# Performance work log

Hardware: AMD Instinct MI355X
Metric: run time of the kernel (lower is better)

## Reference

```python
import jax, jax.numpy as jnp
import numpy as np

ALPHA = 0.01
EPS = 1e-15


def setup_inputs() -> dict:
    key = jax.random.key(0)
    k1, k2, k3, k4 = jax.random.split(key, 4)
    B, C = 65536, 1000
    out = jax.random.normal(k1, (B, C), dtype=jnp.float32)
    correction = jax.random.normal(k2, (C, C), dtype=jnp.float32)
    target = jax.random.randint(k3, (B,), 0, C, dtype=jnp.int64)
    T = jax.random.uniform(k4, (C, C), dtype=jnp.float32)
    return {"out": out, "correction": correction, "target": target, "T": T}


def reference(out, correction, target, T):
    # out: [B, C] logits; correction, T: [C, C]; target: [B]
    B = out.shape[0]
    rows = jnp.arange(B)

    log_p = jax.nn.log_softmax(out, axis=1)      # [B, C]
    p = jnp.exp(log_p)                           # softmax probs [B, C]

    # T_result = T + alpha * correction; out_T[i] = (T_result^T @ p[i]^T)^T = p[i] @ T_result
    T_result = T + ALPHA * correction            # [C, C]
    out_T = p @ T_result                         # [B, C]

    pro1 = p[rows, target]                       # [B]
    pro2 = out_T[rows, target]                   # [B]
    beta = jax.lax.stop_gradient(pro1 / (pro2 + EPS))  # detached reweight factor

    ce = -log_p[rows, target]                    # per-sample cross entropy [B]
    loss = jnp.mean(beta * ce)                   # sum(beta_i * ce_i) / B
    return loss
```

## Files before the change

kernel.cpp:

```cpp
#include <hip/hip_runtime.h>
#include <math.h>

#define ALPHA 0.01f
#define EPS 1e-15f

typedef float f32x4 __attribute__((ext_vector_type(4)));

__global__ __launch_bounds__(256) void build_TrT_kernel(
    const float* __restrict__ T, const float* __restrict__ corr,
    float* __restrict__ TrT, int C, float* __restrict__ out, int out_size) {
  if (blockIdx.x == 0 && blockIdx.y == 0 && threadIdx.y == 0) {
    for (int i = threadIdx.x; i < out_size; i += 32) out[i] = 0.f;
  }
  __shared__ float tile[32][33];
  const int bx = blockIdx.x * 32;
  const int by = blockIdx.y * 32;
  const int tx = threadIdx.x;
  for (int r = threadIdx.y; r < 32; r += blockDim.y) {
    int j = by + r;
    int t = bx + tx;
    if (j < C && t < C)
      tile[r][tx] = T[(size_t)j * C + t] + ALPHA * corr[(size_t)j * C + t];
  }
  __syncthreads();
  for (int r = threadIdx.y; r < 32; r += blockDim.y) {
    int t = bx + r;
    int j = by + tx;
    if (t < C && j < C)
      TrT[(size_t)t * C + j] = tile[tx][r];
  }
}

template <int CT>
__global__ __launch_bounds__(256) void loss_vec4_fast(
    const float* __restrict__ x, const int* __restrict__ target,
    const float* __restrict__ TrT, float* __restrict__ out,
    int B, float invB) {
  constexpr int F4 = CT / 4;
  constexpr int KF = F4 / 64;
  constexpr int REM = F4 - KF * 64;
  constexpr int KTOT = KF + (REM ? 1 : 0);

  const int lane = threadIdx.x & 63;
  const int wave = threadIdx.x >> 6;
  const int wpb = blockDim.x >> 6;
  const int gwave = blockIdx.x * wpb + wave;
  const int nwave = gridDim.x * wpb;

  float acc = 0.f;
  int row = gwave;
  int tnext = (row < B) ? target[row] : 0;
  for (; row < B; row += nwave) {
    const int t = tnext;
    {
      int nr = row + nwave;
      if (nr < B) tnext = target[nr];
    }
    const f32x4* xr = (const f32x4*)(x + (size_t)row * CT);
    const f32x4* tr = (const f32x4*)(TrT + (size_t)t * CT);
    const float xt = x[(size_t)row * CT + t];

    f32x4 v[KTOT], w[KTOT];
#pragma unroll
    for (int k = 0; k < KF; ++k) {
      const int idx = lane + 64 * k;
      v[k] = __builtin_nontemporal_load(xr + idx);
      w[k] = tr[idx];
    }
    if (REM) {
      const int idx = lane + 64 * KF;
      if (lane < REM) {
        v[KF] = __builtin_nontemporal_load(xr + idx);
        w[KF] = tr[idx];
      } else {
        v[KF] = f32x4{-INFINITY, -INFINITY, -INFINITY, -INFINITY};
        w[KF] = f32x4{0.f, 0.f, 0.f, 0.f};
      }
    }

    float se = 0.f, dot = 0.f;
#pragma unroll
    for (int k = 0; k < KTOT; ++k) {
      float e0 = __expf(v[k].x), e1 = __expf(v[k].y);
      float e2 = __expf(v[k].z), e3 = __expf(v[k].w);
      se += (e0 + e1) + (e2 + e3);
      dot += e0 * w[k].x + e1 * w[k].y + e2 * w[k].z + e3 * w[k].w;
    }
#pragma unroll
    for (int off = 32; off > 0; off >>= 1) {
      se += __shfl_xor(se, off, 64);
      dot += __shfl_xor(dot, off, 64);
    }

    const float et = __expf(xt);
    acc += (et / (dot + EPS * se)) * (__logf(se) - xt);
  }

  __shared__ float lacc[8];
  if (lane == 0) lacc[wave] = acc;
  __syncthreads();
  if (threadIdx.x == 0) {
    float s = 0.f;
    for (int i = 0; i < wpb; ++i) s += lacc[i];
    atomicAdd(out, s * invB);
  }
}

__global__ __launch_bounds__(256) void loss_generic_kernel(
    const float* __restrict__ x, const int* __restrict__ target,
    const float* __restrict__ TrT, const float* __restrict__ T,
    const float* __restrict__ corr, int useTrT,
    float* __restrict__ out, int B, int C, float invB) {
  const int lane = threadIdx.x & 63;
  const int wave = threadIdx.x >> 6;
  const int wpb = blockDim.x >> 6;
  const int gwave = blockIdx.x * wpb + wave;
  const int nwave = gridDim.x * wpb;

  float acc = 0.f;
  for (int row = gwave; row < B; row += nwave) {
    const float* xr = x + (size_t)row * C;
    float m = -INFINITY;
    for (int j = lane; j < C; j += 64) m = fmaxf(m, xr[j]);
#pragma unroll
    for (int off = 32; off > 0; off >>= 1) m = fmaxf(m, __shfl_xor(m, off, 64));

    const int t = target[row];
    const float* tr = TrT + (size_t)t * C;
    float se = 0.f, dot = 0.f;
    for (int j = lane; j < C; j += 64) {
      float e = __expf(xr[j] - m);
      float tv = useTrT ? tr[j]
                        : (T[(size_t)j * C + t] + ALPHA * corr[(size_t)j * C + t]);
      se += e;
      dot += e * tv;
    }
#pragma unroll
    for (int off = 32; off > 0; off >>= 1) {
      se += __shfl_xor(se, off, 64);
      dot += __shfl_xor(dot, off, 64);
    }

    const float xt = xr[t];
    const float et = __expf(xt - m);
    const float beta = (et / se) / (dot / se + EPS);
    const float ce = m + logf(se) - xt;
    acc += beta * ce;
  }

  __shared__ float lacc[8];
  if (lane == 0) lacc[wave] = acc;
  __syncthreads();
  if (threadIdx.x == 0) {
    float s = 0.f;
    for (int i = 0; i < wpb; ++i) s += lacc[i];
    atomicAdd(out, s * invB);
  }
}

extern "C" void kernel_launch(void* const* d_in, const int* in_sizes, int n_in,
                              void* d_out, int out_size, void* d_ws, size_t ws_size,
                              hipStream_t stream) {
  const float* logits = (const float*)d_in[0];
  const float* corr   = (const float*)d_in[1];
  const int*   target = (const int*)d_in[2];
  const float* T      = (const float*)d_in[3];

  const int B = in_sizes[2];
  const int C = in_sizes[0] / B;
  float* loss = (float*)d_out;

  float* TrT = (float*)d_ws;
  const bool useTrT = (ws_size >= (size_t)C * C * sizeof(float));
  const float invB = 1.0f / (float)B;
  const int blocks = 2048;

  if (useTrT && C == 1000) {
    dim3 tb(32, 8);
    dim3 tg((C + 31) / 32, (C + 31) / 32);
    build_TrT_kernel<<<tg, tb, 0, stream>>>(T, corr, TrT, C, loss, out_size);
    loss_vec4_fast<1000><<<blocks, 256, 0, stream>>>(logits, target, TrT, loss, B, invB);
  } else {
    hipMemsetAsync(d_out, 0, sizeof(float) * out_size, stream);
    if (useTrT) {
      dim3 tb(32, 8);
      dim3 tg((C + 31) / 32, (C + 31) / 32);
      build_TrT_kernel<<<tg, tb, 0, stream>>>(T, corr, TrT, C, loss, 0);
    }
    loss_generic_kernel<<<blocks, 256, 0, stream>>>(logits, target, TrT, T, corr,
                                                    useTrT ? 1 : 0, loss, B, C, invB);
  }
}
```

Before: 358.6 us.

## Bucket rows by target so each wave reuses one TrT row

```diff
diff --git a/kernel.cpp b/kernel.cpp
--- a/kernel.cpp
+++ b/kernel.cpp
@@ -3,39 +3,86 @@
 
 #define ALPHA 0.01f
 #define EPS 1e-15f
+#define CAP 1024
 
 typedef float f32x4 __attribute__((ext_vector_type(4)));
 
-__global__ __launch_bounds__(256) void build_TrT_kernel(
+
+__global__ __launch_bounds__(256) void build_TrT_init(
     const float* __restrict__ T, const float* __restrict__ corr,
-    float* __restrict__ TrT, int C, float* __restrict__ out, int out_size) {
-  if (blockIdx.x == 0 && blockIdx.y == 0 && threadIdx.y == 0) {
-    for (int i = threadIdx.x; i < out_size; i += 32) out[i] = 0.f;
+    float* __restrict__ TrT, int C, float* __restrict__ out, int out_size,
+    int* __restrict__ cursors, int nbuckets, int* __restrict__ ovf_cnt) {
+  if (blockIdx.x == 0 && blockIdx.y == 0) {
+    int tid = threadIdx.y * 32 + threadIdx.x;
+    for (int i = tid; i < nbuckets; i += 256) cursors[i] = 0;
+    for (int i = tid; i < out_size; i += 256) out[i] = 0.f;
+    if (tid == 0 && ovf_cnt) *ovf_cnt = 0;
   }
   __shared__ float tile[32][33];
-  const int bx = blockIdx.x * 32;
-  const int by = blockIdx.y * 32;
+  const int bx = blockIdx.x * 32, by = blockIdx.y * 32;
   const int tx = threadIdx.x;
   for (int r = threadIdx.y; r < 32; r += blockDim.y) {
-    int j = by + r;
-    int t = bx + tx;
+    int j = by + r, t = bx + tx;
     if (j < C && t < C)
       tile[r][tx] = T[(size_t)j * C + t] + ALPHA * corr[(size_t)j * C + t];
   }
   __syncthreads();
   for (int r = threadIdx.y; r < 32; r += blockDim.y) {
-    int t = bx + r;
-    int j = by + tx;
-    if (t < C && j < C)
-      TrT[(size_t)t * C + j] = tile[tx][r];
-  }
+    int t = bx + r, j = by + tx;
+    if (t < C && j < C) TrT[(size_t)t * C + j] = tile[tx][r];
+  }
+}
+
+__global__ __launch_bounds__(256) void scatter_kernel(
+    const int* __restrict__ target, int B, int* __restrict__ cursors,
+    int* __restrict__ rowlist, int* __restrict__ ovflist,
+    int* __restrict__ ovf_cnt) {
+  int i = blockIdx.x * 256 + threadIdx.x;
+  if (i >= B) return;
+  int t = target[i];
+  int k = atomicAdd(&cursors[t], 1);
+  if (k < CAP) rowlist[(size_t)t * CAP + k] = i;
+  else { int o = atomicAdd(ovf_cnt, 1); ovflist[o] = i; }
+}
+
+template <int CT, int KTOT, int KF, int REM>
+__device__ __forceinline__ float row_term(const float* __restrict__ x,
+                                          int row, int t, const f32x4* wv,
+                                          int lane) {
+  const f32x4* xr = (const f32x4*)(x + (size_t)row * CT);
+  const float xt = x[(size_t)row * CT + t];
+  f32x4 v[KTOT];
+#pragma unroll
+  for (int k = 0; k < KF; ++k)
+    v[k] = __builtin_nontemporal_load(xr + (lane + 64 * k));
+  if (REM) {
+    if (lane < REM) v[KF] = __builtin_nontemporal_load(xr + (lane + 64 * KF));
+    else v[KF] = f32x4{-INFINITY, -INFINITY, -INFINITY, -INFINITY};
+  }
+  float se = 0.f, dot = 0.f;
+#pragma unroll
+  for (int k = 0; k < KTOT; ++k) {
+    float e0 = __expf(v[k].x), e1 = __expf(v[k].y);
+    float e2 = __expf(v[k].z), e3 = __expf(v[k].w);
+    se += (e0 + e1) + (e2 + e3);
+    dot += e0 * wv[k].x + e1 * wv[k].y + e2 * wv[k].z + e3 * wv[k].w;
+  }
+#pragma unroll
+  for (int off = 32; off > 0; off >>= 1) {
+    se += __shfl_xor(se, off, 64);
+    dot += __shfl_xor(dot, off, 64);
+  }
+  const float et = __expf(xt);
+  return (et / (dot + EPS * se)) * (__logf(se) - xt);
 }
 
 template <int CT>
-__global__ __launch_bounds__(256) void loss_vec4_fast(
-    const float* __restrict__ x, const int* __restrict__ target,
-    const float* __restrict__ TrT, float* __restrict__ out,
-    int B, float invB) {
+__global__ __launch_bounds__(256) void loss_bucket(
+    const float* __restrict__ x, const float* __restrict__ TrT,
+    const int* __restrict__ cursors, const int* __restrict__ rowlist,
+    const int* __restrict__ ovflist, const int* __restrict__ ovf_cnt,
+    const int* __restrict__ target, float* __restrict__ out,
+    int nbuckets, float invB) {
   constexpr int F4 = CT / 4;
   constexpr int KF = F4 / 64;
   constexpr int REM = F4 - KF * 64;
@@ -44,65 +91,47 @@
   const int lane = threadIdx.x & 63;
   const int wave = threadIdx.x >> 6;
   const int wpb = blockDim.x >> 6;
-  const int gwave = blockIdx.x * wpb + wave;
-  const int nwave = gridDim.x * wpb;
+  const int gw = __builtin_amdgcn_readfirstlane(blockIdx.x * wpb + wave);
+  const int nw = gridDim.x * wpb;
 
   float acc = 0.f;
-  int row = gwave;
-  int tnext = (row < B) ? target[row] : 0;
-  for (; row < B; row += nwave) {
-    const int t = tnext;
-    {
-      int nr = row + nwave;
-      if (nr < B) tnext = target[nr];
-    }
-    const f32x4* xr = (const f32x4*)(x + (size_t)row * CT);
-    const f32x4* tr = (const f32x4*)(TrT + (size_t)t * CT);
-    const float xt = x[(size_t)row * CT + t];
-
-    f32x4 v[KTOT], w[KTOT];
-#pragma unroll
-    for (int k = 0; k < KF; ++k) {
-      const int idx = lane + 64 * k;
-      v[k] = __builtin_nontemporal_load(xr + idx);
-      w[k] = tr[idx];
-    }
-    if (REM) {
-      const int idx = lane + 64 * KF;
-      if (lane < REM) {
-        v[KF] = __builtin_nontemporal_load(xr + idx);
-        w[KF] = tr[idx];
-      } else {
-        v[KF] = f32x4{-INFINITY, -INFINITY, -INFINITY, -INFINITY};
-        w[KF] = f32x4{0.f, 0.f, 0.f, 0.f};
-      }
-    }
-
-    float se = 0.f, dot = 0.f;
-#pragma unroll
-    for (int k = 0; k < KTOT; ++k) {
-      float e0 = __expf(v[k].x), e1 = __expf(v[k].y);
-      float e2 = __expf(v[k].z), e3 = __expf(v[k].w);
-      se += (e0 + e1) + (e2 + e3);
-      dot += e0 * w[k].x + e1 * w[k].y + e2 * w[k].z + e3 * w[k].w;
-    }
-#pragma unroll
-    for (int off = 32; off > 0; off >>= 1) {
-      se += __shfl_xor(se, off, 64);
-      dot += __shfl_xor(dot, off, 64);
-    }
-
-    const float et = __expf(xt);
-    acc += (et / (dot + EPS * se)) * (__logf(se) - xt);
+  if (gw < nbuckets * 8) {
+    const int b = gw >> 3, s = gw & 7;
+    int count = cursors[b];
+    if (count > CAP) count = CAP;
+    const f32x4* tr = (const f32x4*)(TrT + (size_t)b * CT);
+    f32x4 w[KTOT];
+#pragma unroll
+    for (int k = 0; k < KF; ++k) w[k] = tr[lane + 64 * k];
+    if (REM) w[KF] = (lane < REM) ? tr[lane + 64 * KF] : f32x4{0.f, 0.f, 0.f, 0.f};
+    const int* rl = rowlist + (size_t)b * CAP;
+    for (int k = s; k < count; k += 8) {
+      const int row = rl[k];
+      acc += row_term<CT, KTOT, KF, REM>(x, row, b, w, lane);
+    }
+  } else {
+    const int no = *ovf_cnt;
+    const int widx = gw - nbuckets * 8;
+    const int novw = nw - nbuckets * 8;
+    for (int k = widx; k < no; k += novw) {
+      const int row = ovflist[k];
+      const int t = target[row];
+      const f32x4* tr = (const f32x4*)(TrT + (size_t)t * CT);
+      f32x4 w[KTOT];
+#pragma unroll
+      for (int kk = 0; kk < KF; ++kk) w[kk] = tr[lane + 64 * kk];
+      if (REM) w[KF] = (lane < REM) ? tr[lane + 64 * KF] : f32x4{0.f, 0.f, 0.f, 0.f};
+      acc += row_term<CT, KTOT, KF, REM>(x, row, t, w, lane);
+    }
   }
 
   __shared__ float lacc[8];
   if (lane == 0) lacc[wave] = acc;
   __syncthreads();
   if (threadIdx.x == 0) {
-    float s = 0.f;
-    for (int i = 0; i < wpb; ++i) s += lacc[i];
-    atomicAdd(out, s * invB);
+    float s2 = 0.f;
+    for (int i = 0; i < wpb; ++i) s2 += lacc[i];
+    atomicAdd(out, s2 * invB);
   }
 }
 
@@ -124,7 +153,6 @@
     for (int j = lane; j < C; j += 64) m = fmaxf(m, xr[j]);
 #pragma unroll
     for (int off = 32; off > 0; off >>= 1) m = fmaxf(m, __shfl_xor(m, off, 64));
-
     const int t = target[row];
     const float* tr = TrT + (size_t)t * C;
     float se = 0.f, dot = 0.f;
@@ -140,14 +168,10 @@
       se += __shfl_xor(se, off, 64);
       dot += __shfl_xor(dot, off, 64);
     }
-
     const float xt = xr[t];
     const float et = __expf(xt - m);
-    const float beta = (et / se) / (dot / se + EPS);
-    const float ce = m + logf(se) - xt;
-    acc += beta * ce;
-  }
-
+    acc += (et / se) / (dot / se + EPS) * (m + logf(se) - xt);
+  }
   __shared__ float lacc[8];
   if (lane == 0) lacc[wave] = acc;
   __syncthreads();
@@ -169,25 +193,35 @@
   const int B = in_sizes[2];
   const int C = in_sizes[0] / B;
   float* loss = (float*)d_out;
-
-  float* TrT = (float*)d_ws;
-  const bool useTrT = (ws_size >= (size_t)C * C * sizeof(float));
   const float invB = 1.0f / (float)B;
-  const int blocks = 2048;
-
-  if (useTrT && C == 1000) {
+
+  float* TrT     = (float*)d_ws;
+  int*   cursors = (int*)d_ws + 1000000;
+  int*   ovf_cnt = (int*)d_ws + 1001000;
+  int*   rowlist = (int*)d_ws + 1001024;
+  int*   ovflist = (int*)d_ws + 2025024;
+  const size_t need = (size_t)(2025024 + 65536 + B) * 4;
+
+  if (C == 1000 && ws_size >= need) {
     dim3 tb(32, 8);
     dim3 tg((C + 31) / 32, (C + 31) / 32);
-    build_TrT_kernel<<<tg, tb, 0, stream>>>(T, corr, TrT, C, loss, out_size);
-    loss_vec4_fast<1000><<<blocks, 256, 0, stream>>>(logits, target, TrT, loss, B, invB);
+    build_TrT_init<<<tg, tb, 0, stream>>>(T, corr, TrT, C, loss, out_size,
+                                          cursors, C, ovf_cnt);
+    scatter_kernel<<<(B + 255) / 256, 256, 0, stream>>>(target, B, cursors,
+                                                        rowlist, ovflist, ovf_cnt);
+    loss_bucket<1000><<<2048, 256, 0, stream>>>(logits, TrT, cursors, rowlist,
+                                                ovflist, ovf_cnt, target, loss,
+                                                C, invB);
   } else {
     hipMemsetAsync(d_out, 0, sizeof(float) * out_size, stream);
+    const bool useTrT = (ws_size >= (size_t)C * C * sizeof(float));
     if (useTrT) {
       dim3 tb(32, 8);
       dim3 tg((C + 31) / 32, (C + 31) / 32);
-      build_TrT_kernel<<<tg, tb, 0, stream>>>(T, corr, TrT, C, loss, 0);
-    }
-    loss_generic_kernel<<<blocks, 256, 0, stream>>>(logits, target, TrT, T, corr,
-                                                    useTrT ? 1 : 0, loss, B, C, invB);
-  }
-}
+      build_TrT_init<<<tg, tb, 0, stream>>>(T, corr, TrT, C, loss, 0,
+                                            (int*)nullptr, 0, (int*)nullptr);
+    }
+    loss_generic_kernel<<<2048, 256, 0, stream>>>(logits, target, TrT, T, corr,
+                                                  useTrT ? 1 : 0, loss, B, C, invB);
+  }
+}
```

After: 373.7 us. +4.2%, slower.

## Double-buffer row loads in loss kernel to overlap memory with compute

Applied to the files above, without the earlier changes.

```diff
diff --git a/kernel.cpp b/kernel.cpp
--- a/kernel.cpp
+++ b/kernel.cpp
@@ -6,94 +6,106 @@
 
 typedef float f32x4 __attribute__((ext_vector_type(4)));
 
-__global__ __launch_bounds__(256) void build_TrT_kernel(
+__global__ __launch_bounds__(256) void build_TrT_init(
     const float* __restrict__ T, const float* __restrict__ corr,
     float* __restrict__ TrT, int C, float* __restrict__ out, int out_size) {
-  if (blockIdx.x == 0 && blockIdx.y == 0 && threadIdx.y == 0) {
-    for (int i = threadIdx.x; i < out_size; i += 32) out[i] = 0.f;
+  if (blockIdx.x == 0 && blockIdx.y == 0) {
+    int tid = threadIdx.y * 32 + threadIdx.x;
+    for (int i = tid; i < out_size; i += 256) out[i] = 0.f;
   }
   __shared__ float tile[32][33];
-  const int bx = blockIdx.x * 32;
-  const int by = blockIdx.y * 32;
+  const int bx = blockIdx.x * 32, by = blockIdx.y * 32;
   const int tx = threadIdx.x;
   for (int r = threadIdx.y; r < 32; r += blockDim.y) {
-    int j = by + r;
-    int t = bx + tx;
+    int j = by + r, t = bx + tx;
     if (j < C && t < C)
       tile[r][tx] = T[(size_t)j * C + t] + ALPHA * corr[(size_t)j * C + t];
   }
   __syncthreads();
   for (int r = threadIdx.y; r < 32; r += blockDim.y) {
-    int t = bx + r;
-    int j = by + tx;
-    if (t < C && j < C)
-      TrT[(size_t)t * C + j] = tile[tx][r];
+    int t = bx + r, j = by + tx;
+    if (t < C && j < C) TrT[(size_t)t * C + j] = tile[tx][r];
   }
 }
 
+template <int CT, int KT, int KF, int REM>
+__device__ __forceinline__ void issue_row(const float* __restrict__ x,
+                                          const float* __restrict__ TrT,
+                                          int row, int t, int lane,
+                                          f32x4* v, f32x4* w, float* xt) {
+  const f32x4* xr = (const f32x4*)(x + (size_t)row * CT);
+  const f32x4* tr = (const f32x4*)(TrT + (size_t)t * CT);
+  *xt = x[(size_t)row * CT + t];
+#pragma unroll
+  for (int k = 0; k < KF; ++k) {
+    v[k] = __builtin_nontemporal_load(xr + (lane + 64 * k));
+    w[k] = tr[lane + 64 * k];
+  }
+  if (REM) {
+    if (lane < REM) {
+      v[KF] = __builtin_nontemporal_load(xr + (lane + 64 * KF));
+      w[KF] = tr[lane + 64 * KF];
+    } else {
+      v[KF] = f32x4{-INFINITY, -INFINITY, -INFINITY, -INFINITY};
+      w[KF] = f32x4{0.f, 0.f, 0.f, 0.f};
+    }
+  }
+}
+
+template <int KT>
+__device__ __forceinline__ float row_compute(const f32x4* v, const f32x4* w,
+                                             float xt) {
+  float se = 0.f, dot = 0.f;
+#pragma unroll
+  for (int k = 0; k < KT; ++k) {
+    float e0 = __expf(v[k].x), e1 = __expf(v[k].y);
+    float e2 = __expf(v[k].z), e3 = __expf(v[k].w);
+    se += (e0 + e1) + (e2 + e3);
+    dot += e0 * w[k].x + e1 * w[k].y + e2 * w[k].z + e3 * w[k].w;
+  }
+#pragma unroll
+  for (int off = 32; off > 0; off >>= 1) {
+    se += __shfl_xor(se, off, 64);
+    dot += __shfl_xor(dot, off, 64);
+  }
+  const float et = __expf(xt);
+  return (et / (dot + EPS * se)) * (__logf(se) - xt);
+}
+
 template <int CT>
-__global__ __launch_bounds__(256) void loss_vec4_fast(
+__global__ __launch_bounds__(256, 4) void loss_pipe(
     const float* __restrict__ x, const int* __restrict__ target,
     const float* __restrict__ TrT, float* __restrict__ out,
     int B, float invB) {
   constexpr int F4 = CT / 4;
   constexpr int KF = F4 / 64;
   constexpr int REM = F4 - KF * 64;
-  constexpr int KTOT = KF + (REM ? 1 : 0);
+  constexpr int KT = KF + (REM ? 1 : 0);
 
   const int lane = threadIdx.x & 63;
   const int wave = threadIdx.x >> 6;
   const int wpb = blockDim.x >> 6;
-  const int gwave = blockIdx.x * wpb + wave;
-  const int nwave = gridDim.x * wpb;
+  const int gw = blockIdx.x * wpb + wave;
+  const int nw = gridDim.x * wpb;
 
+  f32x4 vA[KT], wA[KT], vB[KT], wB[KT];
+  float xtA = 0.f, xtB = 0.f;
   float acc = 0.f;
-  int row = gwave;
-  int tnext = (row < B) ? target[row] : 0;
-  for (; row < B; row += nwave) {
-    const int t = tnext;
-    {
-      int nr = row + nwave;
-      if (nr < B) tnext = target[nr];
-    }
-    const f32x4* xr = (const f32x4*)(x + (size_t)row * CT);
-    const f32x4* tr = (const f32x4*)(TrT + (size_t)t * CT);
-    const float xt = x[(size_t)row * CT + t];
 
-    f32x4 v[KTOT], w[KTOT];
-#pragma unroll
-    for (int k = 0; k < KF; ++k) {
-      const int idx = lane + 64 * k;
-      v[k] = __builtin_nontemporal_load(xr + idx);
-      w[k] = tr[idx];
-    }
-    if (REM) {
-      const int idx = lane + 64 * KF;
-      if (lane < REM) {
-        v[KF] = __builtin_nontemporal_load(xr + idx);
-        w[KF] = tr[idx];
-      } else {
-        v[KF] = f32x4{-INFINITY, -INFINITY, -INFINITY, -INFINITY};
-        w[KF] = f32x4{0.f, 0.f, 0.f, 0.f};
-      }
-    }
+  int rA = gw;
+  int rB = gw + nw;
+  if (rA < B) issue_row<CT, KT, KF, REM>(x, TrT, rA, target[rA], lane, vA, wA, &xtA);
+  if (rB < B) issue_row<CT, KT, KF, REM>(x, TrT, rB, target[rB], lane, vB, wB, &xtB);
 
-    float se = 0.f, dot = 0.f;
-#pragma unroll
-    for (int k = 0; k < KTOT; ++k) {
-      float e0 = __expf(v[k].x), e1 = __expf(v[k].y);
-      float e2 = __expf(v[k].z), e3 = __expf(v[k].w);
-      se += (e0 + e1) + (e2 + e3);
-      dot += e0 * w[k].x + e1 * w[k].y + e2 * w[k].z + e3 * w[k].w;
-    }
-#pragma unroll
-    for (int off = 32; off > 0; off >>= 1) {
-      se += __shfl_xor(se, off, 64);
-      dot += __shfl_xor(dot, off, 64);
-    }
-
-    const float et = __expf(xt);
-    acc += (et / (dot + EPS * se)) * (__logf(se) - xt);
+  while (rA < B) {
+    acc += row_compute<KT>(vA, wA, xtA);
+    const int rA2 = rA + 2 * nw;
+    if (rA2 < B) issue_row<CT, KT, KF, REM>(x, TrT, rA2, target[rA2], lane, vA, wA, &xtA);
+    if (rB < B) acc += row_compute<KT>(vB, wB, xtB);
+    const int rB2 = rB + 2 * nw;
+    if (rB2 < B) issue_row<CT, KT, KF, REM>(x, TrT, rB2, target[rB2], lane, vB, wB, &xtB);
+    rA = rA2;
+    rB = rB2;
   }
 
   __shared__ float lacc[8];
@@ -124,7 +136,6 @@
     for (int j = lane; j < C; j += 64) m = fmaxf(m, xr[j]);
 #pragma unroll
     for (int off = 32; off > 0; off >>= 1) m = fmaxf(m, __shfl_xor(m, off, 64));
-
     const int t = target[row];
     const float* tr = TrT + (size_t)t * C;
     float se = 0.f, dot = 0.f;
@@ -140,14 +151,10 @@
       se += __shfl_xor(se, off, 64);
       dot += __shfl_xor(dot, off, 64);
     }
-
     const float xt = xr[t];
     const float et = __expf(xt - m);
-    const float beta = (et / se) / (dot / se + EPS);
-    const float ce = m + logf(se) - xt;
-    acc += beta * ce;
+    acc += (et / se) / (dot / se + EPS) * (m + logf(se) - xt);
   }
-
   __shared__ float lacc[8];
   if (lane == 0) lacc[wave] = acc;
   __syncthreads();
@@ -169,25 +176,24 @@
   const int B = in_sizes[2];
   const int C = in_sizes[0] / B;
   float* loss = (float*)d_out;
+  const float invB = 1.0f / (float)B;
 
   float* TrT = (float*)d_ws;
   const bool useTrT = (ws_size >= (size_t)C * C * sizeof(float));
-  const float invB = 1.0f / (float)B;
-  const int blocks = 2048;
 
   if (useTrT && C == 1000) {
     dim3 tb(32, 8);
     dim3 tg((C + 31) / 32, (C + 31) / 32);
-    build_TrT_kernel<<<tg, tb, 0, stream>>>(T, corr, TrT, C, loss, out_size);
-    loss_vec4_fast<1000><<<blocks, 256, 0, stream>>>(logits, target, TrT, loss, B, invB);
+    build_TrT_init<<<tg, tb, 0, stream>>>(T, corr, TrT, C, loss, out_size);
+    loss_pipe<1000><<<1024, 256, 0, stream>>>(logits, target, TrT, loss, B, invB);
   } else {
     hipMemsetAsync(d_out, 0, sizeof(float) * out_size, stream);
     if (useTrT) {
       dim3 tb(32, 8);
       dim3 tg((C + 31) / 32, (C + 31) / 32);
-      build_TrT_kernel<<<tg, tb, 0, stream>>>(T, corr, TrT, C, loss, 0);
+      build_TrT_init<<<tg, tb, 0, stream>>>(T, corr, TrT, C, loss, 0);
     }
-    loss_generic_kernel<<<blocks, 256, 0, stream>>>(logits, target, TrT, T, corr,
-                                                    useTrT ? 1 : 0, loss, B, C, invB);
+    loss_generic_kernel<<<2048, 256, 0, stream>>>(logits, target, TrT, T, corr,
+                                                  useTrT ? 1 : 0, loss, B, C, invB);
   }
 }
```

Measured after the change: 357.9 us. Within noise of the previous version (-0.2%).
